# Kernel tuning notes

Measured on AMD Instinct MI355X. Metric: run time of the kernel, lower is better.

## Reference

```python
import jax, jax.numpy as jnp
import numpy as np

N_QUBITS = 12
N_LAYERS = 3
HID = 16
IN_DIM = 6
BATCH = 4096
C64 = jnp.complex64


def _ry(t):
    c = jnp.cos(t / 2).astype(C64)
    s = jnp.sin(t / 2).astype(C64)
    return jnp.stack([jnp.stack([c, -s], -1), jnp.stack([s, c], -1)], -2)


def _rx(t):
    c = jnp.cos(t / 2).astype(C64)
    s = jnp.sin(t / 2).astype(C64)
    js = 1j * s
    return jnp.stack([jnp.stack([c, -js], -1), jnp.stack([-js, c], -1)], -2)


def _rz(t):
    e = jnp.exp(-1j * t.astype(C64) / 2)
    z = jnp.zeros_like(e)
    return jnp.stack([jnp.stack([e, z], -1), jnp.stack([z, jnp.conj(e)], -1)], -2)


def _apply_1q(state, U, wire):
    # state: (B,) + (2,)*n ; U: (2,2) shared or (B,2,2) per-sample
    s = jnp.moveaxis(state, wire + 1, 1)
    if U.ndim == 2:
        s = jnp.einsum('ij,bj...->bi...', U, s)
    else:
        s = jnp.einsum('bij,bj...->bi...', U, s)
    return jnp.moveaxis(s, 1, wire + 1)


def _cnot(state, c, t):
    ax_c = c + 1
    s0 = jnp.take(state, 0, axis=ax_c)
    s1 = jnp.take(state, 1, axis=ax_c)
    t_ax = t + 1 if t < c else t  # target axis after removing control axis
    s1 = jnp.flip(s1, axis=t_ax)  # X on target when control=1
    return jnp.stack([s0, s1], axis=ax_c)


def _quantum(angles, qparams):
    # angles: (B, n_qubits) angle-encoding RY rotations; qparams: (L, n, 3)
    B = angles.shape[0]
    n = N_QUBITS
    state = jnp.zeros((B,) + (2,) * n, C64).at[(slice(None),) + (0,) * n].set(1.0)
    for i in range(n):
        state = _apply_1q(state, _ry(angles[:, i]), i)
    for l in range(N_LAYERS):
        for i in range(n):
            # RX then RY then RZ on wire i -> fused 2x2
            U = _rz(qparams[l, i, 2]) @ _ry(qparams[l, i, 1]) @ _rx(qparams[l, i, 0])
            state = _apply_1q(state, U, i)
        for i in range(n - 1):
            state = _cnot(state, i, i + 1)
        if n > 2:
            state = _cnot(state, n - 1, 0)
    p = state.real ** 2 + state.imag ** 2  # (B,) + (2,)*n
    evs = []
    for i in range(n):
        axes = tuple(a for a in range(1, n + 1) if a != i + 1)
        pi = p.sum(axes)  # (B, 2)
        evs.append(pi[:, 0] - pi[:, 1])
    return jnp.stack(evs, axis=1)  # (B, n) PauliZ expvals


def setup_inputs() -> dict:
    key = jax.random.key(0)
    ks = jax.random.split(key, 14)
    w = lambda k, shape: jax.random.normal(k, shape, jnp.float32) * 0.1
    return {
        'x': jax.random.normal(ks[0], (BATCH, IN_DIM), jnp.float32),
        'W1': w(ks[1], (HID, IN_DIM)), 'b1': w(ks[2], (HID,)),
        'W2': w(ks[3], (HID, HID)), 'b2': w(ks[4], (HID,)),
        'W3': w(ks[5], (N_QUBITS, HID)), 'b3': w(ks[6], (N_QUBITS,)),
        'qparams': w(ks[7], (N_LAYERS, N_QUBITS, 3)),
        'P1': w(ks[8], (HID, N_QUBITS)), 'c1': w(ks[9], (HID,)),
        'P2': w(ks[10], (8, HID)), 'c2': w(ks[11], (8,)),
        'P3': w(ks[12], (1, 8)), 'c3': w(ks[13], (1,)),
    }


def reference(x, W1, b1, W2, b2, W3, b3, qparams, P1, c1, P2, c2, P3, c3):
    # classical preprocessor (dropout = identity at inference)
    h = jax.nn.relu(x @ W1.T + b1)
    h = jax.nn.relu(h @ W2.T + b2)
    angles = h @ W3.T + b3  # (B, n_qubits)
    q = _quantum(angles, qparams)  # (B, n_qubits)
    # classical postprocessor
    o = jax.nn.relu(q @ P1.T + c1)
    o = jax.nn.relu(o @ P2.T + c2)
    o = jax.nn.sigmoid(o @ P3.T + c3)
    return o.squeeze(-1)  # (B,)
```

## Files before the change

kernel.cpp:

```cpp
#include <hip/hip_runtime.h>
#include <stdint.h>

#define NQ   12
#define DIM  4096
#define TPB  256

typedef float   v2f   __attribute__((ext_vector_type(2)));
typedef float   v4f   __attribute__((ext_vector_type(4)));
typedef float   f32x4 __attribute__((ext_vector_type(4)));
typedef _Float16 v2h  __attribute__((ext_vector_type(2)));
typedef _Float16 f16x8 __attribute__((ext_vector_type(8)));
typedef uint32_t u32x4 __attribute__((ext_vector_type(4)));


constexpr int par(uint32_t x) { return __builtin_popcount(x) & 1; }
constexpr int chbit(uint32_t x) { int b=-1; for (int i=0;i<32;++i) if ((x>>i)&1u) b=i; return b; }

constexpr void bmm(uint32_t* C, const uint32_t* A, const uint32_t* B) {
  for (int i = 0; i < NQ; ++i) {
    uint32_t r = 0;
    for (int j = 0; j < NQ; ++j) if ((A[i] >> j) & 1u) r ^= B[j];
    C[i] = r;
  }
}
constexpr void binv(const uint32_t* M, uint32_t* Inv) {
  uint32_t A[NQ] = {}, I[NQ] = {};
  for (int i = 0; i < NQ; ++i) { A[i] = M[i]; I[i] = 1u << i; }
  for (int c = 0; c < NQ; ++c) {
    int piv = -1;
    for (int r = c; r < NQ; ++r) if ((A[r] >> c) & 1u) { piv = r; break; }
    if (piv < 0) continue;
    uint32_t ta = A[c]; A[c] = A[piv]; A[piv] = ta;
    uint32_t ti = I[c]; I[c] = I[piv]; I[piv] = ti;
    for (int r = 0; r < NQ; ++r)
      if (r != c && ((A[r] >> c) & 1u)) { A[r] ^= A[c]; I[r] ^= I[c]; }
  }
  for (int i = 0; i < NQ; ++i) Inv[i] = I[i];
}

constexpr void pass_v(int p, uint32_t* v) {
  uint32_t A[NQ] = {}; A[0] = 0xFFEu;
  for (int i = 1; i < NQ; ++i) A[i] = (1u << (i + 1)) - 1u;
  uint32_t A2[NQ] = {}, Ai[NQ] = {}, A2i[NQ] = {};
  bmm(A2, A, A); binv(A, Ai); binv(A2, A2i);
  const uint32_t* Mi = (p < 3) ? Ai : A2i;
  const int wb = (p % 3) * 4;
  for (int i = 0; i < 4; ++i) {
    uint32_t col = 0;
    for (int r = 0; r < NQ; ++r) col |= ((Mi[r] >> (wb + i)) & 1u) << r;
    v[i] = col;
  }
}

constexpr bool addvec(uint32_t* red, uint32_t x) {
  while (x) {
    const int h = chbit(x);
    if (red[h]) x ^= red[h]; else { red[h] = x; return true; }
  }
  return false;
}
constexpr bool tryindep(const uint32_t* red, uint32_t x) {
  uint32_t tmp[16] = {};
  for (int i = 0; i < 16; ++i) tmp[i] = red[i];
  return addvec(tmp, x);
}

struct B12 { uint32_t d[12]; };
struct LC  { B12 b; uint32_t mi[12]; uint32_t G[12]; };

constexpr B12 make_basis(int p) {
  B12 b{};
  uint32_t v[4] = {}; pass_v(p, v);
  uint32_t red[16] = {};
  addvec(red, v[0]); addvec(red, v[1]); addvec(red, v[2]); addvec(red, v[3]);
  b.d[0] = v[0]; b.d[1] = v[1]; b.d[6] = v[2]; b.d[7] = v[3];
  const int slots[8] = {2, 3, 4, 5, 8, 9, 10, 11};
  int si = 0;
  if (p > 0) {
    uint32_t pv[4] = {}; pass_v(p - 1, pv);
    if (addvec(red, pv[0])) b.d[slots[si++]] = pv[0];
    if (addvec(red, pv[3])) b.d[slots[si++]] = pv[3];
  }
  for (int e = 0; e < 12 && si < 8; ++e)
    if (addvec(red, 1u << e)) b.d[slots[si++]] = 1u << e;
  return b;
}

constexpr uint32_t lapc(const LC& lc, uint32_t y) {
  uint32_t r = 0;
  for (int bb = 0; bb < 12; ++bb) r |= (uint32_t)par(lc.mi[bb] & y) << bb;
  return r;
}

constexpr uint32_t rowbits(const uint32_t* V, int nv, int b) {
  uint32_t r = 0;
  for (int k = 0; k < nv; ++k) r |= ((V[k] >> b) & 1u) << k;
  return r;
}

constexpr void solve_sig(const uint32_t* V, int nv, bool incl2, uint32_t* Cm) {
  uint32_t red[16] = {};
  addvec(red, rowbits(V, nv, 0));
  addvec(red, rowbits(V, nv, 1));
  int bs[3] = {}; int nbs = 0;
  if (incl2) bs[nbs++] = 2;
  bs[nbs++] = 3; bs[nbs++] = 4;
  for (int bi = 0; bi < nbs; ++bi) {
    const int b = bs[bi];
    uint32_t r = rowbits(V, nv, b);
    Cm[b] = 0;
    if (addvec(red, r)) continue;
    bool done = false;
    for (int h = 5; h < 12 && !done; ++h) {
      uint32_t cand = r ^ rowbits(V, nv, h);
      if (tryindep(red, cand)) { addvec(red, cand); Cm[b] = 1u << h; done = true; }
    }
    for (int h1 = 5; h1 < 12 && !done; ++h1)
      for (int h2 = h1 + 1; h2 < 12 && !done; ++h2) {
        uint32_t cand = r ^ rowbits(V, nv, h1) ^ rowbits(V, nv, h2);
        if (tryindep(red, cand)) { addvec(red, cand); Cm[b] = (1u << h1) | (1u << h2); done = true; }
      }
  }
}

constexpr LC make_lc(int p) {
  LC lc{};
  lc.b = make_basis(p);
  uint32_t Mr[NQ] = {};
  for (int i = 0; i < NQ; ++i) {
    uint32_t r = 0;
    for (int j = 0; j < NQ; ++j) r |= ((lc.b.d[j] >> i) & 1u) << j;
    Mr[i] = r;
  }
  binv(Mr, lc.mi);
  uint32_t V[6] = {}; bool incl2 = false;
  if (p == 0) {
    for (int k = 0; k < 6; ++k) V[k] = lapc(lc, 1u << k);
    incl2 = true;
  } else {
    B12 pb = make_basis(p - 1);
    V[0] = lapc(lc, pb.d[2]); V[1] = lapc(lc, pb.d[3]);
    V[2] = lapc(lc, pb.d[4]); V[3] = lapc(lc, pb.d[5]);
    V[4] = lapc(lc, pb.d[1]); V[5] = lapc(lc, pb.d[6]);
    incl2 = false;
  }
  uint32_t Cm[5] = {};
  solve_sig(V, 6, incl2, Cm);
  for (int h = 5; h < 12; ++h) {
    uint32_t g = 0;
    for (int b = 2; b < 5; ++b) g |= ((Cm[b] >> h) & 1u) << b;
    lc.G[h] = g;
  }
  return lc;
}

constexpr uint32_t sig_of(const LC& lc, uint32_t x) {
  uint32_t s = 0;
  for (int h = 5; h < 12; ++h) if ((x >> h) & 1u) s ^= lc.G[h];
  return s;
}
constexpr uint32_t img(const LC& lc, uint32_t y) {
  const uint32_t l = lapc(lc, y);
  return l ^ sig_of(lc, l);
}

struct PCon {
  uint32_t G5, G6, G7, G10, G11;
  uint32_t RT[4];
  uint32_t WN[4], WQ1, WQ2, WW0, WW1, WT_[4];
  uint32_t WV0, WV3;
  int      W2;
  uint32_t SM[12]; uint32_t robin[12];
  uint8_t  layer, wb;
};

constexpr PCon make_pcon(int p) {
  PCon c{};
  const LC lp = make_lc(p);
  c.G5 = lp.G[5]; c.G6 = lp.G[6]; c.G7 = lp.G[7]; c.G10 = lp.G[10]; c.G11 = lp.G[11];
  for (int T = 0; T < 4; ++T)
    c.RT[T] = (uint32_t)(T << 8) ^ ((T & 1) ? lp.G[8] : 0) ^ ((T & 2) ? lp.G[9] : 0);
  c.layer = (uint8_t)((p < 3) ? 1 : 2);
  c.wb = (uint8_t)((p % 3) * 4);
  if (p < 5) {
    const LC ln = make_lc(p + 1);
    for (int k = 0; k < 4; ++k) c.WN[k] = img(ln, lp.b.d[2 + k]);
    c.WQ1 = img(ln, lp.b.d[1]); c.WQ2 = img(ln, lp.b.d[6]);
    c.WW0 = img(ln, lp.b.d[10]); c.WW1 = img(ln, lp.b.d[11]);
    const uint32_t wt0 = img(ln, lp.b.d[8]), wt1 = img(ln, lp.b.d[9]);
    for (int T = 0; T < 4; ++T) c.WT_[T] = ((T & 1) ? wt0 : 0) ^ ((T & 2) ? wt1 : 0);
    c.WV0 = img(ln, lp.b.d[0]); c.WV3 = img(ln, lp.b.d[7]);
    c.W2 = (c.WV0 == 4u && c.WV3 == 8u) ? 1 : 0;
  } else {
    uint32_t A[NQ] = {}; A[0] = 0xFFEu;
    for (int i = 1; i < NQ; ++i) A[i] = (1u << (i + 1)) - 1u;
    uint32_t A2[NQ] = {}, A3[NQ] = {};
    bmm(A2, A, A); bmm(A3, A2, A);
    for (int i = 0; i < NQ; ++i) {
      uint32_t sm = 0;
      sm |= (uint32_t)par(A3[i] & lp.b.d[2])  << 0;
      sm |= (uint32_t)par(A3[i] & lp.b.d[3])  << 1;
      sm |= (uint32_t)par(A3[i] & lp.b.d[4])  << 2;
      sm |= (uint32_t)par(A3[i] & lp.b.d[5])  << 3;
      sm |= (uint32_t)par(A3[i] & lp.b.d[1])  << 4;
      sm |= (uint32_t)par(A3[i] & lp.b.d[6])  << 5;
      sm |= (uint32_t)par(A3[i] & lp.b.d[10]) << 6;
      sm |= (uint32_t)par(A3[i] & lp.b.d[11]) << 7;
      c.SM[i] = sm;
      c.robin[i] = (uint32_t)par(A3[i] & lp.b.d[0])
                 | (uint32_t)par(A3[i] & lp.b.d[7]) << 1
                 | (uint32_t)par(A3[i] & lp.b.d[8]) << 2
                 | (uint32_t)par(A3[i] & lp.b.d[9]) << 3;
    }
  }
  return c;
}

constexpr PCon PC0 = make_pcon(0);
constexpr PCon PC1 = make_pcon(1);
constexpr PCon PC2 = make_pcon(2);
constexpr PCon PC3 = make_pcon(3);
constexpr PCon PC4 = make_pcon(4);
constexpr PCon PC5 = make_pcon(5);

template<int P> constexpr PCon pget() {
  if constexpr (P == 0) return PC0;
  else if constexpr (P == 1) return PC1;
  else if constexpr (P == 2) return PC2;
  else if constexpr (P == 3) return PC3;
  else if constexpr (P == 4) return PC4;
  else return PC5;
}

struct InitC { uint32_t ICt[8]; uint32_t ICj[16]; };
constexpr InitC make_init() {
  InitC ic{};
  const LC l0 = make_lc(0);
  for (int b = 0; b < 8; ++b) ic.ICt[b] = img(l0, 1u << b);
  uint32_t Jc[4] = {};
  for (int b = 0; b < 4; ++b) Jc[b] = img(l0, 1u << (8 + b));
  for (int j = 0; j < 16; ++j) {
    uint32_t r = 0;
    for (int b = 0; b < 4; ++b) if ((j >> b) & 1) r ^= Jc[b];
    ic.ICj[j] = r;
  }
  return ic;
}
constexpr InitC IC = make_init();

__device__ __forceinline__ v2f cmulf(v2f a, v2f b) {
  return (v2f){a.x * b.x - a.y * b.y, a.x * b.y + a.y * b.x};
}
__device__ __forceinline__ uint32_t f2h2(float a, float b) {
  return __builtin_bit_cast(uint32_t, __builtin_amdgcn_cvt_pkrtz(a, b));
}
__device__ __forceinline__ uint32_t pk_rtn(float a, float b) {
  v2h h = {(_Float16)a, (_Float16)b};
  return __builtin_bit_cast(uint32_t, h);
}
__device__ __forceinline__ void build_u(const float* __restrict__ qp, int l, int w, float U[8]) {
  float p0 = qp[(l * 12 + w) * 3 + 0];
  float p1 = qp[(l * 12 + w) * 3 + 1];
  float p2 = qp[(l * 12 + w) * 3 + 2];
  float cx, sx, cy, sy, cz, sz;
  sincosf(0.5f * p0, &sx, &cx);
  sincosf(0.5f * p1, &sy, &cy);
  sincosf(0.5f * p2, &sz, &cz);
  float M00x =  cy * cx, M00y =  sy * sx;
  float M01x = -sy * cx, M01y = -cy * sx;
  float M10x =  sy * cx, M10y = -cy * sx;
  float M11x =  cy * cx, M11y = -sy * sx;
  U[0] = cz * M00x + sz * M00y; U[1] = cz * M00y - sz * M00x;
  U[2] = cz * M01x + sz * M01y; U[3] = cz * M01y - sz * M01x;
  U[4] = cz * M10x - sz * M10y; U[5] = cz * M10y + sz * M10x;
  U[6] = cz * M11x - sz * M11y; U[7] = cz * M11y + sz * M11x;
}
__device__ __forceinline__ int am_col(int c, int i) {
  return ((((c >> 2) ^ ((i >> 1) & 3)) << 2) | (c & 3));
}

template<int P>
__device__ __forceinline__ void build_am_g(uint32_t* __restrict__ Am_g,
                                           const v2f (*gg)[12][4], int t) {
  constexpr PCon pc = pget<P>();
  const int r_ = t >> 4, c_ = t & 15;
  v2f e = (v2f){1.f, 0.f};
  #pragma unroll
  for (int i = 0; i < 4; ++i) {
    v2f u = gg[pc.layer - 1][pc.wb + i][(((r_ >> i) & 1) << 1) | ((c_ >> i) & 1)];
    e = cmulf(e, u);
  }
  const int ra = 2 * r_, rb = 2 * r_ + 1;
  Am_g[P * 512 + ra * 16 + am_col(c_, ra)] = pk_rtn(e.x, -e.y);
  Am_g[P * 512 + rb * 16 + am_col(c_, rb)] = pk_rtn(e.y, e.x);
}

__global__ __launch_bounds__(256) void prep_kernel(const float* __restrict__ qp,
                                                   uint32_t* __restrict__ Am_g,
                                                   float* __restrict__ U0_g) {
  __shared__ v2f gg[2][12][4];
  const int t = threadIdx.x;
  if (t < 24) {
    const int L = t / 12 + 1, w = t % 12;
    float U[8]; build_u(qp, L, w, U);
    gg[L - 1][w][0] = (v2f){U[0], U[1]};
    gg[L - 1][w][1] = (v2f){U[2], U[3]};
    gg[L - 1][w][2] = (v2f){U[4], U[5]};
    gg[L - 1][w][3] = (v2f){U[6], U[7]};
  } else if (t >= 32 && t < 44) {
    const int w = t - 32;
    float U[8]; build_u(qp, 0, w, U);
    #pragma unroll
    for (int k = 0; k < 8; ++k) U0_g[w * 8 + k] = U[k];
  }
  __syncthreads();
  build_am_g<0>(Am_g, gg, t);
  build_am_g<1>(Am_g, gg, t);
  build_am_g<2>(Am_g, gg, t);
  build_am_g<3>(Am_g, gg, t);
  build_am_g<4>(Am_g, gg, t);
  build_am_g<5>(Am_g, gg, t);
}

template<int P, bool LAST>
__device__ __forceinline__ void do_pass(uint32_t* st, f16x8 a0, f16x8 a1,
                                        int lane, int wvl, float* ev) {
  constexpr PCon pc = pget<P>();
  const int n = lane & 15, q = lane >> 4;
  const int rb = (n << 2) ^ ((n >> 3) ? pc.G5 : 0)
               ^ (q << 6) ^ ((q & 1) ? pc.G6 : 0) ^ ((q & 2) ? pc.G7 : 0)
               ^ (wvl << 10) ^ ((wvl & 1) ? pc.G10 : 0) ^ ((wvl & 2) ? pc.G11 : 0);
  int wb_ = 0;
  if constexpr (!LAST) {
    wb_ = ((n & 1) ? pc.WN[0] : 0) ^ ((n & 2) ? pc.WN[1] : 0)
        ^ ((n & 4) ? pc.WN[2] : 0) ^ ((n & 8) ? pc.WN[3] : 0)
        ^ ((q & 1) ? pc.WQ1 : 0)   ^ ((q & 2) ? pc.WQ2 : 0)
        ^ ((wvl & 1) ? pc.WW0 : 0) ^ ((wvl & 2) ? pc.WW1 : 0);
  }
  float pr[16];
  const f32x4 z = {0.f, 0.f, 0.f, 0.f};
  #pragma unroll
  for (int T = 0; T < 4; ++T) {
    u32x4 braw = *reinterpret_cast<const u32x4*>(&st[rb ^ pc.RT[T]]);
    f16x8 bf = __builtin_bit_cast(f16x8, braw);
    f32x4 c0 = __builtin_amdgcn_mfma_f32_16x16x32_f16(a0, bf, z, 0, 0, 0);
    f32x4 c1 = __builtin_amdgcn_mfma_f32_16x16x32_f16(a1, bf, z, 0, 0, 0);
    if constexpr (!LAST) {
      const int A = wb_ ^ pc.WT_[T];
      uint32_t w00 = f2h2(c0.x, c0.y), w10 = f2h2(c0.z, c0.w);
      uint32_t w01 = f2h2(c1.x, c1.y), w11 = f2h2(c1.z, c1.w);
      if constexpr (pc.W2) {
        const bool b2 = (A >> 2) & 1;
        const int base0 = A & ~4;
        const int base1 = base0 ^ 8;
        st[base0]     = b2 ? w10 : w00;
        st[base0 + 4] = b2 ? w00 : w10;
        st[base1]     = b2 ? w11 : w01;
        st[base1 + 4] = b2 ? w01 : w11;
      } else {
        st[A]                        = w00;
        st[A ^ pc.WV0]               = w10;
        st[A ^ pc.WV3]               = w01;
        st[A ^ (pc.WV0 ^ pc.WV3)]    = w11;
      }
    } else {
      const int nb = ((T & 1) << 2) | ((T >> 1) << 3);
      pr[nb]     = c0.x * c0.x + c0.y * c0.y;
      pr[nb | 1] = c0.z * c0.z + c0.w * c0.w;
      pr[nb | 2] = c1.x * c1.x + c1.y * c1.y;
      pr[nb | 3] = c1.z * c1.z + c1.w * c1.w;
    }
  }
  if constexpr (LAST) {
    #pragma unroll
    for (int gs = 1; gs < 16; gs <<= 1) {
      #pragma unroll
      for (int j = 0; j < 16; ++j) {
        if (j & gs) continue;
        float u = pr[j], w2 = pr[j | gs];
        pr[j] = u + w2; pr[j | gs] = u - w2;
      }
    }
    const int pw = n | (q << 4) | (wvl << 6);
    #pragma unroll
    for (int i = 0; i < NQ; ++i) {
      float h = pr[pc.robin[i]];
      int s = (__popc((int)pc.SM[i] & pw) & 1) << 31;
      ev[i] = __int_as_float(__float_as_int(h) ^ s);
    }
  }
}

#define LDA(P, A0, A1) {                                                        \
  const int li_ = lane & 15;                                                    \
  const int q_  = (lane >> 4) ^ ((li_ >> 1) & 3);                               \
  A0 = __builtin_bit_cast(f16x8,                                                \
      *reinterpret_cast<const u32x4*>(Am_g + (P) * 512 + li_ * 16 + q_ * 4));   \
  A1 = __builtin_bit_cast(f16x8,                                                \
      *reinterpret_cast<const u32x4*>(Am_g + (P) * 512 + (li_ + 16) * 16 + q_ * 4)); \
}

__global__ __launch_bounds__(TPB, 8) void hqc_kernel(
    const float* __restrict__ x,  const float* __restrict__ W1, const float* __restrict__ b1,
    const float* __restrict__ W2, const float* __restrict__ b2,
    const float* __restrict__ W3, const float* __restrict__ b3,
    const float* __restrict__ P1, const float* __restrict__ c1,
    const float* __restrict__ P2, const float* __restrict__ c2,
    const float* __restrict__ P3, const float* __restrict__ c3,
    const uint32_t* __restrict__ Am_g, const float* __restrict__ U0_g,
    float* __restrict__ out)
{
  __shared__ __align__(16) uint32_t st[DIM];
  __shared__ v4f  gpk0[12][2];
  __shared__ float red[4][NQ];

  const int s    = blockIdx.x;
  const int t    = threadIdx.x;
  const int lane = t & 63;
  const int wv   = t >> 6;

  f16x8 a0c, a1c, a0n, a1n;
  LDA(0, a0c, a1c)

  if (wv == 0 && lane < 16) {
    float a = b1[lane];
    #pragma unroll
    for (int k = 0; k < 6; ++k) a = fmaf(W1[lane * 6 + k], x[s * 6 + k], a);
    float h1 = fmaxf(a, 0.f);
    float a2 = b2[lane];
    #pragma unroll
    for (int k = 0; k < 16; ++k) a2 = fmaf(W2[lane * 16 + k], __shfl(h1, k, 64), a2);
    float h2 = fmaxf(a2, 0.f);
    const int lw = (lane < NQ) ? lane : 0;
    float a3 = b3[lw];
    #pragma unroll
    for (int k = 0; k < 16; ++k) a3 = fmaf(W3[lw * 16 + k], __shfl(h2, k, 64), a3);
    if (lane < NQ) {
      const float* u = U0_g + lane * 8;
      float ca, sa; sincosf(0.5f * a3, &sa, &ca);
      float c0x = u[0] * ca + u[2] * sa, c0y = u[1] * ca + u[3] * sa;
      float c1x = u[4] * ca + u[6] * sa, c1y = u[5] * ca + u[7] * sa;
      gpk0[lane][0] = (v4f){c0x, c0x, -c0y, c0y};
      gpk0[lane][1] = (v4f){c1x, c1x, -c1y, c1y};
    }
  }
  __syncthreads();

  {
    int tb = 0;
    #pragma unroll
    for (int b = 0; b < 8; ++b) if ((t >> b) & 1) tb ^= IC.ICt[b];
    v2f acc = (v2f){1.f, 0.f};
    #pragma unroll
    for (int i = 0; i < 8; ++i) {
      v4f gk = gpk0[i][(t >> i) & 1];
      acc = gk.xy * acc + gk.zw * acc.yx;
    }
    v2f l16[16];
    l16[0] = acc;
    #pragma unroll
    for (int i = 0; i < 4; ++i) {
      v4f g0 = gpk0[8 + i][0], g1 = gpk0[8 + i][1];
      #pragma unroll
      for (int j = 0; j < (1 << i); ++j) {
        v2f a = l16[j];
        l16[j | (1 << i)] = g1.xy * a + g1.zw * a.yx;
        l16[j]            = g0.xy * a + g0.zw * a.yx;
      }
    }
    #pragma unroll
    for (int j = 0; j < 16; ++j) st[tb ^ IC.ICj[j]] = f2h2(l16[j].x, l16[j].y);
  }
  __syncthreads();

  float ev[NQ];
  LDA(1, a0n, a1n)
  do_pass<0, false>(st, a0c, a1c, lane, wv, ev); __syncthreads();
  a0c = a0n; a1c = a1n; LDA(2, a0n, a1n)
  do_pass<1, false>(st, a0c, a1c, lane, wv, ev); __syncthreads();
  a0c = a0n; a1c = a1n; LDA(3, a0n, a1n)
  do_pass<2, false>(st, a0c, a1c, lane, wv, ev); __syncthreads();
  a0c = a0n; a1c = a1n; LDA(4, a0n, a1n)
  do_pass<3, false>(st, a0c, a1c, lane, wv, ev); __syncthreads();
  a0c = a0n; a1c = a1n; LDA(5, a0n, a1n)
  do_pass<4, false>(st, a0c, a1c, lane, wv, ev); __syncthreads();
  a0c = a0n; a1c = a1n;
  do_pass<5, true >(st, a0c, a1c, lane, wv, ev);

  #pragma unroll
  for (int off = 32; off >= 1; off >>= 1) {
    #pragma unroll
    for (int i = 0; i < NQ; ++i) ev[i] += __shfl_xor(ev[i], off, 64);
  }
  if (lane == 0) {
    #pragma unroll
    for (int i = 0; i < NQ; ++i) red[wv][i] = ev[i];
  }
  __syncthreads();

  if (wv == 0 && lane < 16) {
    float q = (lane < NQ)
      ? (red[0][lane] + red[1][lane] + red[2][lane] + red[3][lane])
      : 0.f;
    float a = c1[lane];
    #pragma unroll
    for (int j = 0; j < NQ; ++j) a = fmaf(P1[lane * NQ + j], __shfl(q, j, 64), a);
    float o1 = fmaxf(a, 0.f);
    float a2 = c2[lane & 7];
    #pragma unroll
    for (int j = 0; j < 16; ++j) a2 = fmaf(P2[(lane & 7) * 16 + j], __shfl(o1, j, 64), a2);
    float o2 = fmaxf(a2, 0.f);
    float a3 = c3[0];
    #pragma unroll
    for (int j = 0; j < 8; ++j) a3 = fmaf(P3[j], __shfl(o2, j, 64), a3);
    if (lane == 0) out[s] = 1.f / (1.f + expf(-a3));
  }
}

extern "C" void kernel_launch(void* const* d_in, const int* in_sizes, int n_in,
                              void* d_out, int out_size, void* d_ws, size_t ws_size,
                              hipStream_t stream) {
  (void)in_sizes; (void)n_in; (void)ws_size;
  uint32_t* Am_g = (uint32_t*)d_ws;
  float*    U0_g = (float*)((char*)d_ws + 6 * 512 * 4);
  const float* qp = (const float*)d_in[7];
  prep_kernel<<<1, 256, 0, stream>>>(qp, Am_g, U0_g);
  hqc_kernel<<<out_size, TPB, 0, stream>>>(
      (const float*)d_in[0],  (const float*)d_in[1],  (const float*)d_in[2],
      (const float*)d_in[3],  (const float*)d_in[4],  (const float*)d_in[5],
      (const float*)d_in[6],
      (const float*)d_in[8],  (const float*)d_in[9],
      (const float*)d_in[10], (const float*)d_in[11],
      (const float*)d_in[12], (const float*)d_in[13],
      Am_g, U0_g,
      (float*)d_out);
}
```

Before: 58.69 us.

## Rework compile-time basis choice to enable linear reads and 128-bit state writes

```diff
diff --git a/kernel.cpp b/kernel.cpp
--- a/kernel.cpp
+++ b/kernel.cpp
@@ -38,17 +38,18 @@
   for (int i = 0; i < NQ; ++i) Inv[i] = I[i];
 }
 
-constexpr void pass_v(int p, uint32_t* v) {
+constexpr void pass_vm(int p, uint32_t* v, uint32_t* m) {
   uint32_t A[NQ] = {}; A[0] = 0xFFEu;
   for (int i = 1; i < NQ; ++i) A[i] = (1u << (i + 1)) - 1u;
   uint32_t A2[NQ] = {}, Ai[NQ] = {}, A2i[NQ] = {};
   bmm(A2, A, A); binv(A, Ai); binv(A2, A2i);
+  const uint32_t* M  = (p < 3) ? A  : A2;
   const uint32_t* Mi = (p < 3) ? Ai : A2i;
   const int wb = (p % 3) * 4;
   for (int i = 0; i < 4; ++i) {
     uint32_t col = 0;
     for (int r = 0; r < NQ; ++r) col |= ((Mi[r] >> (wb + i)) & 1u) << r;
-    v[i] = col;
+    v[i] = col; m[i] = M[wb + i];
   }
 }
 
@@ -59,169 +60,182 @@
   }
   return false;
 }
-constexpr bool tryindep(const uint32_t* red, uint32_t x) {
-  uint32_t tmp[16] = {};
-  for (int i = 0; i < 16; ++i) tmp[i] = red[i];
-  return addvec(tmp, x);
-}
-
-struct B12 { uint32_t d[12]; };
-struct LC  { B12 b; uint32_t mi[12]; uint32_t G[12]; };
-
-constexpr B12 make_basis(int p) {
-  B12 b{};
-  uint32_t v[4] = {}; pass_v(p, v);
+constexpr int rankbits(const uint32_t* w, int n) {
+  uint32_t red[8] = {}; int r = 0;
+  for (int q = 0; q < n; ++q) {
+    uint32_t x = w[q];
+    while (x) {
+      const int h = chbit(x);
+      if (red[h]) x ^= red[h]; else { red[h] = x; ++r; break; }
+    }
+  }
+  return r;
+}
+constexpr void perm_decode(int idx, int* s) {
+  int avail[6] = {0, 1, 2, 3, 4, 5};
+  const int f[6] = {120, 24, 6, 2, 1, 1};
+  for (int i = 0; i < 6; ++i) {
+    const int k = idx / f[i]; idx %= f[i];
+    s[i] = avail[k];
+    for (int j = k; j < 5 - i; ++j) avail[j] = avail[j + 1];
+  }
+}
+
+struct Lay { uint32_t d[12]; uint32_t mi[12]; int tok; };
+
+constexpr Lay make_lay(int p, const Lay& prev, bool hasPrev) {
+  Lay L{};
+  uint32_t v[4] = {}, m[4] = {};
+  pass_vm(p, v, m);
+  L.d[0] = v[0]; L.d[1] = v[1]; L.d[6] = v[2]; L.d[7] = v[3];
   uint32_t red[16] = {};
   addvec(red, v[0]); addvec(red, v[1]); addvec(red, v[2]); addvec(red, v[3]);
-  b.d[0] = v[0]; b.d[1] = v[1]; b.d[6] = v[2]; b.d[7] = v[3];
-  const int slots[8] = {2, 3, 4, 5, 8, 9, 10, 11};
-  int si = 0;
-  if (p > 0) {
-    uint32_t pv[4] = {}; pass_v(p - 1, pv);
-    if (addvec(red, pv[0])) b.d[slots[si++]] = pv[0];
-    if (addvec(red, pv[3])) b.d[slots[si++]] = pv[3];
-  }
-  for (int e = 0; e < 12 && si < 8; ++e)
-    if (addvec(red, 1u << e)) b.d[slots[si++]] = 1u << e;
-  return b;
-}
-
-constexpr uint32_t lapc(const LC& lc, uint32_t y) {
-  uint32_t r = 0;
-  for (int bb = 0; bb < 12; ++bb) r |= (uint32_t)par(lc.mi[bb] & y) << bb;
-  return r;
-}
-
-constexpr uint32_t rowbits(const uint32_t* V, int nv, int b) {
-  uint32_t r = 0;
-  for (int k = 0; k < nv; ++k) r |= ((V[k] >> b) & 1u) << k;
-  return r;
-}
-
-constexpr void solve_sig(const uint32_t* V, int nv, bool incl2, uint32_t* Cm) {
-  uint32_t red[16] = {};
-  addvec(red, rowbits(V, nv, 0));
-  addvec(red, rowbits(V, nv, 1));
-  int bs[3] = {}; int nbs = 0;
-  if (incl2) bs[nbs++] = 2;
-  bs[nbs++] = 3; bs[nbs++] = 4;
-  for (int bi = 0; bi < nbs; ++bi) {
-    const int b = bs[bi];
-    uint32_t r = rowbits(V, nv, b);
-    Cm[b] = 0;
-    if (addvec(red, r)) continue;
-    bool done = false;
-    for (int h = 5; h < 12 && !done; ++h) {
-      uint32_t cand = r ^ rowbits(V, nv, h);
-      if (tryindep(red, cand)) { addvec(red, cand); Cm[b] = 1u << h; done = true; }
-    }
-    for (int h1 = 5; h1 < 12 && !done; ++h1)
-      for (int h2 = h1 + 1; h2 < 12 && !done; ++h2) {
-        uint32_t cand = r ^ rowbits(V, nv, h1) ^ rowbits(V, nv, h2);
-        if (tryindep(red, cand)) { addvec(red, cand); Cm[b] = (1u << h1) | (1u << h2); done = true; }
+  L.tok = 0;
+  if (p < 5) {
+    uint32_t vn[4] = {}, mn[4] = {};
+    pass_vm(p + 1, vn, mn);
+    bool roles0 = true;
+    for (int i = 0; i < 4; ++i)
+      if (par(m[i] & vn[0]) || par(m[i] & vn[1])) roles0 = false;
+    if (roles0) {
+      uint32_t tmp[16] = {};
+      for (int i = 0; i < 16; ++i) tmp[i] = red[i];
+      if (addvec(tmp, vn[0]) && addvec(tmp, vn[1])) {
+        addvec(red, vn[0]); addvec(red, vn[1]);
+        L.d[8] = vn[0]; L.d[9] = vn[1]; L.tok = 1;
       }
-  }
-}
-
-constexpr LC make_lc(int p) {
-  LC lc{};
-  lc.b = make_basis(p);
-  uint32_t Mr[NQ] = {};
+    }
+  }
+  uint32_t pool[8] = {}; int np = 0;
+  const int need = L.tok ? 6 : 8;
+  for (int b = 0; b < 12 && np < need; ++b) {
+    uint32_t cand = 1u << b;
+    for (int i = 0; i < 4; ++i) if ((m[i] >> b) & 1u) cand ^= v[i];
+    if (addvec(red, cand)) pool[np++] = cand;
+  }
+  if (!L.tok) { L.d[8] = pool[6]; L.d[9] = pool[7]; }
+  const int S[6] = {2, 3, 4, 5, 10, 11};
+  for (int i = 0; i < 6; ++i) L.d[S[i]] = pool[i];
+  uint32_t Mr[NQ] = {}, miC[NQ] = {};
   for (int i = 0; i < NQ; ++i) {
     uint32_t r = 0;
-    for (int j = 0; j < NQ; ++j) r |= ((lc.b.d[j] >> i) & 1u) << j;
+    for (int j = 0; j < NQ; ++j) r |= ((L.d[j] >> i) & 1u) << j;
     Mr[i] = r;
   }
-  binv(Mr, lc.mi);
-  uint32_t V[6] = {}; bool incl2 = false;
-  if (p == 0) {
-    for (int k = 0; k < 6; ++k) V[k] = lapc(lc, 1u << k);
-    incl2 = true;
+  binv(Mr, miC);
+  uint32_t V[8] = {}; int nv = 0; int mode5 = 1;
+  if (!hasPrev) {
+    for (int k = 0; k < 8; ++k) {
+      uint32_t c = 0;
+      for (int bb = 0; bb < 12; ++bb) c |= (uint32_t)par(miC[bb] & (1u << k)) << bb;
+      V[nv++] = c;
+    }
+    mode5 = 1;
   } else {
-    B12 pb = make_basis(p - 1);
-    V[0] = lapc(lc, pb.d[2]); V[1] = lapc(lc, pb.d[3]);
-    V[2] = lapc(lc, pb.d[4]); V[3] = lapc(lc, pb.d[5]);
-    V[4] = lapc(lc, pb.d[1]); V[5] = lapc(lc, pb.d[6]);
-    incl2 = false;
-  }
-  uint32_t Cm[5] = {};
-  solve_sig(V, 6, incl2, Cm);
-  for (int h = 5; h < 12; ++h) {
-    uint32_t g = 0;
-    for (int b = 2; b < 5; ++b) g |= ((Cm[b] >> h) & 1u) << b;
-    lc.G[h] = g;
-  }
-  return lc;
-}
-
-constexpr uint32_t sig_of(const LC& lc, uint32_t x) {
-  uint32_t s = 0;
-  for (int h = 5; h < 12; ++h) if ((x >> h) & 1u) s ^= lc.G[h];
-  return s;
-}
-constexpr uint32_t img(const LC& lc, uint32_t y) {
-  const uint32_t l = lapc(lc, y);
-  return l ^ sig_of(lc, l);
+    const uint32_t src[6] = {prev.d[2], prev.d[3], prev.d[4], prev.d[5],
+                             prev.d[1], prev.d[6]};
+    for (int k = 0; k < 6; ++k) {
+      uint32_t c = 0;
+      for (int bb = 0; bb < 12; ++bb) c |= (uint32_t)par(miC[bb] & src[k]) << bb;
+      V[nv++] = c;
+    }
+    mode5 = prev.tok ? 0 : 1;
+  }
+  int bestP = 0, bestSc = -1;
+  for (int pi = 0; pi < 720; ++pi) {
+    int sg[6] = {}; perm_decode(pi, sg);
+    uint32_t pw[8] = {};
+    for (int k = 0; k < nv; ++k) {
+      uint32_t w = 0;
+      if (mode5) {
+        w |= V[k] & 3u;
+        for (int i = 0; i < 3; ++i)
+          w |= (uint32_t)((V[k] >> S[sg[i]]) & 1u) << (2 + i);
+      } else {
+        for (int i = 0; i < 3; ++i)
+          w |= (uint32_t)((V[k] >> S[sg[i]]) & 1u) << i;
+      }
+      pw[k] = w;
+    }
+    const int sc = rankbits(pw, nv);
+    if (sc > bestSc) { bestSc = sc; bestP = pi; }
+  }
+  int sg[6] = {}; perm_decode(bestP, sg);
+  for (int i = 0; i < 6; ++i) L.d[S[i]] = pool[sg[i]];
+  for (int i = 0; i < NQ; ++i) {
+    uint32_t r = 0;
+    for (int j = 0; j < NQ; ++j) r |= ((L.d[j] >> i) & 1u) << j;
+    Mr[i] = r;
+  }
+  binv(Mr, L.mi);
+  return L;
+}
+
+constexpr Lay LY0 = make_lay(0, Lay{}, false);
+constexpr Lay LY1 = make_lay(1, LY0, true);
+constexpr Lay LY2 = make_lay(2, LY1, true);
+constexpr Lay LY3 = make_lay(3, LY2, true);
+constexpr Lay LY4 = make_lay(4, LY3, true);
+constexpr Lay LY5 = make_lay(5, LY4, true);
+
+constexpr uint32_t imgL(const Lay& l, uint32_t y) {
+  uint32_t r = 0;
+  for (int b = 0; b < 12; ++b) r |= (uint32_t)par(l.mi[b] & y) << b;
+  return r;
 }
 
 struct PCon {
-  uint32_t G5, G6, G7, G10, G11;
-  uint32_t RT[4];
-  uint32_t WN[4], WQ1, WQ2, WW0, WW1, WT_[4];
+  uint32_t WN[4], WQ1, WQ2, WW0, WW1;
   uint32_t WV0, WV3;
-  int      W2;
-  uint32_t SM[12]; uint32_t robin[12];
+  uint32_t WT0, WT1;
+  int      W4;
+  uint32_t SM[12], robin[12];
   uint8_t  layer, wb;
 };
 
-constexpr PCon make_pcon(int p) {
+constexpr PCon make_pcon(const Lay& lp, const Lay& ln, int p) {
   PCon c{};
-  const LC lp = make_lc(p);
-  c.G5 = lp.G[5]; c.G6 = lp.G[6]; c.G7 = lp.G[7]; c.G10 = lp.G[10]; c.G11 = lp.G[11];
-  for (int T = 0; T < 4; ++T)
-    c.RT[T] = (uint32_t)(T << 8) ^ ((T & 1) ? lp.G[8] : 0) ^ ((T & 2) ? lp.G[9] : 0);
-  c.layer = (uint8_t)((p < 3) ? 1 : 2);
-  c.wb = (uint8_t)((p % 3) * 4);
-  if (p < 5) {
-    const LC ln = make_lc(p + 1);
-    for (int k = 0; k < 4; ++k) c.WN[k] = img(ln, lp.b.d[2 + k]);
-    c.WQ1 = img(ln, lp.b.d[1]); c.WQ2 = img(ln, lp.b.d[6]);
-    c.WW0 = img(ln, lp.b.d[10]); c.WW1 = img(ln, lp.b.d[11]);
-    const uint32_t wt0 = img(ln, lp.b.d[8]), wt1 = img(ln, lp.b.d[9]);
-    for (int T = 0; T < 4; ++T) c.WT_[T] = ((T & 1) ? wt0 : 0) ^ ((T & 2) ? wt1 : 0);
-    c.WV0 = img(ln, lp.b.d[0]); c.WV3 = img(ln, lp.b.d[7]);
-    c.W2 = (c.WV0 == 4u && c.WV3 == 8u) ? 1 : 0;
-  } else {
-    uint32_t A[NQ] = {}; A[0] = 0xFFEu;
-    for (int i = 1; i < NQ; ++i) A[i] = (1u << (i + 1)) - 1u;
-    uint32_t A2[NQ] = {}, A3[NQ] = {};
-    bmm(A2, A, A); bmm(A3, A2, A);
-    for (int i = 0; i < NQ; ++i) {
-      uint32_t sm = 0;
-      sm |= (uint32_t)par(A3[i] & lp.b.d[2])  << 0;
-      sm |= (uint32_t)par(A3[i] & lp.b.d[3])  << 1;
-      sm |= (uint32_t)par(A3[i] & lp.b.d[4])  << 2;
-      sm |= (uint32_t)par(A3[i] & lp.b.d[5])  << 3;
-      sm |= (uint32_t)par(A3[i] & lp.b.d[1])  << 4;
-      sm |= (uint32_t)par(A3[i] & lp.b.d[6])  << 5;
-      sm |= (uint32_t)par(A3[i] & lp.b.d[10]) << 6;
-      sm |= (uint32_t)par(A3[i] & lp.b.d[11]) << 7;
-      c.SM[i] = sm;
-      c.robin[i] = (uint32_t)par(A3[i] & lp.b.d[0])
-                 | (uint32_t)par(A3[i] & lp.b.d[7]) << 1
-                 | (uint32_t)par(A3[i] & lp.b.d[8]) << 2
-                 | (uint32_t)par(A3[i] & lp.b.d[9]) << 3;
-    }
-  }
+  c.layer = (uint8_t)((p < 3) ? 1 : 2); c.wb = (uint8_t)((p % 3) * 4);
+  for (int k = 0; k < 4; ++k) c.WN[k] = imgL(ln, lp.d[2 + k]);
+  c.WQ1 = imgL(ln, lp.d[1]);  c.WQ2 = imgL(ln, lp.d[6]);
+  c.WW0 = imgL(ln, lp.d[10]); c.WW1 = imgL(ln, lp.d[11]);
+  c.WV0 = imgL(ln, lp.d[0]);  c.WV3 = imgL(ln, lp.d[7]);
+  c.WT0 = imgL(ln, lp.d[8]);  c.WT1 = imgL(ln, lp.d[9]);
+  c.W4 = (lp.tok && c.WT0 == 1u && c.WT1 == 2u) ? 1 : 0;
   return c;
 }
-
-constexpr PCon PC0 = make_pcon(0);
-constexpr PCon PC1 = make_pcon(1);
-constexpr PCon PC2 = make_pcon(2);
-constexpr PCon PC3 = make_pcon(3);
-constexpr PCon PC4 = make_pcon(4);
-constexpr PCon PC5 = make_pcon(5);
+constexpr PCon make_pcon5(const Lay& lp) {
+  PCon c{};
+  c.layer = 2; c.wb = 8; c.W4 = 0;
+  uint32_t A[NQ] = {}; A[0] = 0xFFEu;
+  for (int i = 1; i < NQ; ++i) A[i] = (1u << (i + 1)) - 1u;
+  uint32_t A2[NQ] = {}, A3[NQ] = {};
+  bmm(A2, A, A); bmm(A3, A2, A);
+  for (int i = 0; i < NQ; ++i) {
+    uint32_t sm = 0;
+    sm |= (uint32_t)par(A3[i] & lp.d[2])  << 0;
+    sm |= (uint32_t)par(A3[i] & lp.d[3])  << 1;
+    sm |= (uint32_t)par(A3[i] & lp.d[4])  << 2;
+    sm |= (uint32_t)par(A3[i] & lp.d[5])  << 3;
+    sm |= (uint32_t)par(A3[i] & lp.d[1])  << 4;
+    sm |= (uint32_t)par(A3[i] & lp.d[6])  << 5;
+    sm |= (uint32_t)par(A3[i] & lp.d[10]) << 6;
+    sm |= (uint32_t)par(A3[i] & lp.d[11]) << 7;
+    c.SM[i] = sm;
+    c.robin[i] = (uint32_t)par(A3[i] & lp.d[0])
+               | (uint32_t)par(A3[i] & lp.d[7]) << 1
+               | (uint32_t)par(A3[i] & lp.d[8]) << 2
+               | (uint32_t)par(A3[i] & lp.d[9]) << 3;
+  }
+  return c;
+}
+
+constexpr PCon PC0 = make_pcon(LY0, LY1, 0);
+constexpr PCon PC1 = make_pcon(LY1, LY2, 1);
+constexpr PCon PC2 = make_pcon(LY2, LY3, 2);
+constexpr PCon PC3 = make_pcon(LY3, LY4, 3);
+constexpr PCon PC4 = make_pcon(LY4, LY5, 4);
+constexpr PCon PC5 = make_pcon5(LY5);
 
 template<int P> constexpr PCon pget() {
   if constexpr (P == 0) return PC0;
@@ -235,10 +249,9 @@
 struct InitC { uint32_t ICt[8]; uint32_t ICj[16]; };
 constexpr InitC make_init() {
   InitC ic{};
-  const LC l0 = make_lc(0);
-  for (int b = 0; b < 8; ++b) ic.ICt[b] = img(l0, 1u << b);
+  for (int b = 0; b < 8; ++b) ic.ICt[b] = imgL(LY0, 1u << b);
   uint32_t Jc[4] = {};
-  for (int b = 0; b < 4; ++b) Jc[b] = img(l0, 1u << (8 + b));
+  for (int b = 0; b < 4; ++b) Jc[b] = imgL(LY0, 1u << (8 + b));
   for (int j = 0; j < 16; ++j) {
     uint32_t r = 0;
     for (int b = 0; b < 4; ++b) if ((j >> b) & 1) r ^= Jc[b];
@@ -327,9 +340,7 @@
                                         int lane, int wvl, float* ev) {
   constexpr PCon pc = pget<P>();
   const int n = lane & 15, q = lane >> 4;
-  const int rb = (n << 2) ^ ((n >> 3) ? pc.G5 : 0)
-               ^ (q << 6) ^ ((q & 1) ? pc.G6 : 0) ^ ((q & 2) ? pc.G7 : 0)
-               ^ (wvl << 10) ^ ((wvl & 1) ? pc.G10 : 0) ^ ((wvl & 2) ? pc.G11 : 0);
+  const int rb = (n << 2) | (q << 6) | (wvl << 10);
   int wb_ = 0;
   if constexpr (!LAST) {
     wb_ = ((n & 1) ? pc.WN[0] : 0) ^ ((n & 2) ? pc.WN[1] : 0)
@@ -337,41 +348,58 @@
         ^ ((q & 1) ? pc.WQ1 : 0)   ^ ((q & 2) ? pc.WQ2 : 0)
         ^ ((wvl & 1) ? pc.WW0 : 0) ^ ((wvl & 2) ? pc.WW1 : 0);
   }
-  float pr[16];
   const f32x4 z = {0.f, 0.f, 0.f, 0.f};
-  #pragma unroll
-  for (int T = 0; T < 4; ++T) {
-    u32x4 braw = *reinterpret_cast<const u32x4*>(&st[rb ^ pc.RT[T]]);
-    f16x8 bf = __builtin_bit_cast(f16x8, braw);
-    f32x4 c0 = __builtin_amdgcn_mfma_f32_16x16x32_f16(a0, bf, z, 0, 0, 0);
-    f32x4 c1 = __builtin_amdgcn_mfma_f32_16x16x32_f16(a1, bf, z, 0, 0, 0);
-    if constexpr (!LAST) {
-      const int A = wb_ ^ pc.WT_[T];
-      uint32_t w00 = f2h2(c0.x, c0.y), w10 = f2h2(c0.z, c0.w);
-      uint32_t w01 = f2h2(c1.x, c1.y), w11 = f2h2(c1.z, c1.w);
-      if constexpr (pc.W2) {
-        const bool b2 = (A >> 2) & 1;
-        const int base0 = A & ~4;
-        const int base1 = base0 ^ 8;
-        st[base0]     = b2 ? w10 : w00;
-        st[base0 + 4] = b2 ? w00 : w10;
-        st[base1]     = b2 ? w11 : w01;
-        st[base1 + 4] = b2 ? w01 : w11;
-      } else {
-        st[A]                        = w00;
-        st[A ^ pc.WV0]               = w10;
-        st[A ^ pc.WV3]               = w01;
-        st[A ^ (pc.WV0 ^ pc.WV3)]    = w11;
-      }
-    } else {
+  if constexpr (!LAST && pc.W4) {
+    uint32_t wbuf[4][4];
+    #pragma unroll
+    for (int T = 0; T < 4; ++T) {
+      u32x4 braw = *reinterpret_cast<const u32x4*>(&st[rb ^ (T << 8)]);
+      f16x8 bf = __builtin_bit_cast(f16x8, braw);
+      f32x4 c0 = __builtin_amdgcn_mfma_f32_16x16x32_f16(a0, bf, z, 0, 0, 0);
+      f32x4 c1 = __builtin_amdgcn_mfma_f32_16x16x32_f16(a1, bf, z, 0, 0, 0);
+      wbuf[0][T] = f2h2(c0.x, c0.y);
+      wbuf[1][T] = f2h2(c0.z, c0.w);
+      wbuf[2][T] = f2h2(c1.x, c1.y);
+      wbuf[3][T] = f2h2(c1.z, c1.w);
+    }
+    #pragma unroll
+    for (int c = 0; c < 4; ++c) {
+      const int A = wb_ ^ ((c & 1) ? pc.WV0 : 0) ^ ((c & 2) ? pc.WV3 : 0);
+      const bool s0 = A & 1, s1 = A & 2;
+      uint32_t x0 = wbuf[c][0], x1 = wbuf[c][1], x2 = wbuf[c][2], x3 = wbuf[c][3];
+      uint32_t y0 = s0 ? x1 : x0, y1 = s0 ? x0 : x1;
+      uint32_t y2 = s0 ? x3 : x2, y3 = s0 ? x2 : x3;
+      uint32_t z0 = s1 ? y2 : y0, z1 = s1 ? y3 : y1;
+      uint32_t z2 = s1 ? y0 : y2, z3 = s1 ? y1 : y3;
+      *reinterpret_cast<u32x4*>(&st[A & ~3]) = (u32x4){z0, z1, z2, z3};
+    }
+  } else if constexpr (!LAST) {
+    #pragma unroll
+    for (int T = 0; T < 4; ++T) {
+      u32x4 braw = *reinterpret_cast<const u32x4*>(&st[rb ^ (T << 8)]);
+      f16x8 bf = __builtin_bit_cast(f16x8, braw);
+      f32x4 c0 = __builtin_amdgcn_mfma_f32_16x16x32_f16(a0, bf, z, 0, 0, 0);
+      f32x4 c1 = __builtin_amdgcn_mfma_f32_16x16x32_f16(a1, bf, z, 0, 0, 0);
+      const int A = wb_ ^ ((T & 1) ? pc.WT0 : 0) ^ ((T & 2) ? pc.WT1 : 0);
+      st[A]                      = f2h2(c0.x, c0.y);
+      st[A ^ pc.WV0]             = f2h2(c0.z, c0.w);
+      st[A ^ pc.WV3]             = f2h2(c1.x, c1.y);
+      st[A ^ (pc.WV0 ^ pc.WV3)]  = f2h2(c1.z, c1.w);
+    }
+  } else {
+    float pr[16];
+    #pragma unroll
+    for (int T = 0; T < 4; ++T) {
+      u32x4 braw = *reinterpret_cast<const u32x4*>(&st[rb ^ (T << 8)]);
+      f16x8 bf = __builtin_bit_cast(f16x8, braw);
+      f32x4 c0 = __builtin_amdgcn_mfma_f32_16x16x32_f16(a0, bf, z, 0, 0, 0);
+      f32x4 c1 = __builtin_amdgcn_mfma_f32_16x16x32_f16(a1, bf, z, 0, 0, 0);
       const int nb = ((T & 1) << 2) | ((T >> 1) << 3);
       pr[nb]     = c0.x * c0.x + c0.y * c0.y;
       pr[nb | 1] = c0.z * c0.z + c0.w * c0.w;
       pr[nb | 2] = c1.x * c1.x + c1.y * c1.y;
       pr[nb | 3] = c1.z * c1.z + c1.w * c1.w;
     }
-  }
-  if constexpr (LAST) {
     #pragma unroll
     for (int gs = 1; gs < 16; gs <<= 1) {
       #pragma unroll
```

Measured after the change: 48.89 us. -16.7%, faster.
